# Performance work log

Hardware: AMD Instinct MI355X
Metric: run time of the kernel (lower is better)

Reference implementation:

```python
import jax, jax.numpy as jnp
import numpy as np

NUM_KEYPOINTS = 17
MAX_PEOPLE = 30
HEAT_THRESH = 0.1
KERNEL = 3  # NMS max-pool window
STRIDE_SCALE = 4  # heatmap -> image coordinate scale


def setup_inputs() -> dict:
    key = jax.random.key(0)
    # [B, C, H, W] keypoint heatmaps (values in [0,1), thresh=0.1)
    heatmaps = jax.random.uniform(key, (32, NUM_KEYPOINTS, 256, 256), dtype=jnp.float32)
    return {"heatmaps": heatmaps}


def reference(heatmaps):
    """Batched equivalent of PosePostProcessor: max-pool NMS + threshold + top-k.

    Returns fixed-shape (padded) results instead of variable-length Python lists:
      kps:    [B, C, MAX_PEOPLE, 2] int32, (x, y) * 4 image coords (sorted by score desc)
      scores: [B, C, MAX_PEOPLE] float32, 0 where invalid
      valid:  [B, C, MAX_PEOPLE] bool, True where score > heat_thresh
    """
    B, C, H, W = heatmaps.shape
    # 3x3 stride-1 SAME max pool (NMS): keep only local maxima
    hmax = jax.lax.reduce_window(
        heatmaps, -jnp.inf, jax.lax.max,
        window_dimensions=(1, 1, KERNEL, KERNEL),
        window_strides=(1, 1, 1, 1),
        padding="SAME",
    )
    nms = jnp.where(hmax == heatmaps, heatmaps, jnp.zeros((), heatmaps.dtype))
    # per (b, c) top-k over flattened spatial dims; suppress sub-threshold peaks
    flat = nms.reshape(B, C, H * W)
    masked = jnp.where(flat > HEAT_THRESH, flat, -jnp.inf)
    scores, idx = jax.lax.top_k(masked, MAX_PEOPLE)  # [B, C, K]
    x = (idx % W) * STRIDE_SCALE
    y = (idx // W) * STRIDE_SCALE
    kps = jnp.stack([x, y], axis=-1).astype(jnp.int32)  # [B, C, K, 2]
    valid = scores > HEAT_THRESH
    scores = jnp.where(valid, scores, jnp.zeros((), scores.dtype))
    return kps, scores, valid
```

## Files before the change

### kernel.cpp

```cpp
#include <hip/hip_runtime.h>
#include <cstdint>

#define HEAT_THRESH 0.1f
#define STATIC_T 0.998f
#define WW 256
#define HH 256
#define TOPK 30
#define CAPQ 128
#define NBINS 2048
#define CAP2 512
#define BASEBITS 0x3DCCCCCDu
#define BINSH 14
#define MAXBIN 1740

typedef unsigned long long u64;

__device__ __forceinline__ u64 umax64(u64 a, u64 b) { return a > b ? a : b; }

__global__ __launch_bounds__(256, 4) void nms_scan(const float* __restrict__ heat,
                                                   u64* __restrict__ cand,
                                                   int* __restrict__ cntq) {
    const int blk = blockIdx.x;
    const int slice = blk >> 2;
    const int q = blk & 3;
    const float* __restrict__ hm = heat + (size_t)slice * (HH * WW);
    const int tid = threadIdx.x;
    const int lane = tid & 63;
    const int x0 = lane * 4;
    const int y0 = q * 64 + (tid >> 6) * 16;
    const float NEG = -INFINITY;
    const float4 NEG4 = make_float4(NEG, NEG, NEG, NEG);

    __shared__ u64 cl[CAPQ];
    __shared__ int lcnt;
    if (tid == 0) lcnt = 0;
    __syncthreads();

    auto hmaxs = [&](const float4& v, float4& h) {
        float l = __shfl_up(v.w, 1u, 64);
        float r = __shfl_down(v.x, 1u, 64);
        if (lane == 0) l = NEG;
        if (lane == 63) r = NEG;
        h.x = fmaxf(fmaxf(l, v.x), v.y);
        h.y = fmaxf(fmaxf(v.x, v.y), v.z);
        h.z = fmaxf(fmaxf(v.y, v.z), v.w);
        h.w = fmaxf(fmaxf(v.z, v.w), r);
    };

    float4 r[18];
    #pragma unroll
    for (int j = 0; j < 18; ++j) {
        int y = y0 - 1 + j;
        y = (y < 0) ? 0 : ((y > HH - 1) ? HH - 1 : y);
        r[j] = *reinterpret_cast<const float4*>(hm + y * WW + x0);
    }
    __builtin_amdgcn_sched_barrier(0);
    if (y0 == 0)       r[0]  = NEG4;
    if (y0 + 16 == HH) r[17] = NEG4;

    float4 h0, h1, h2;
    hmaxs(r[0], h0);
    hmaxs(r[1], h1);
    #pragma unroll
    for (int t = 0; t < 16; ++t) {
        hmaxs(r[t + 2], h2);
        const float4 c = r[t + 1];
        const float va0 = fmaxf(fmaxf(h0.x, h1.x), h2.x);
        const float va1 = fmaxf(fmaxf(h0.y, h1.y), h2.y);
        const float va2 = fmaxf(fmaxf(h0.z, h1.z), h2.z);
        const float va3 = fmaxf(fmaxf(h0.w, h1.w), h2.w);
        const int ib = (y0 + t) * WW + x0;
        #define PUSH(cv, va, off)                                                       \
            if ((cv) == (va) && (cv) >= STATIC_T) {                                     \
                int p = atomicAdd(&lcnt, 1);                                            \
                if (p < CAPQ)                                                           \
                    cl[p] = ((u64)__float_as_uint(cv) << 32) |                          \
                            (u64)(0xFFFFu - (unsigned)(ib + (off)));                    \
            }
        PUSH(c.x, va0, 0)
        PUSH(c.y, va1, 1)
        PUSH(c.z, va2, 2)
        PUSH(c.w, va3, 3)
        #undef PUSH
        h0 = h1; h1 = h2;
    }
    __syncthreads();

    const int n = lcnt;
    if (tid == 0) cntq[blk] = n;
    const int nf = min(n, CAPQ);
    for (int i = tid; i < nf; i += 256) cand[(size_t)blk * CAPQ + i] = cl[i];
}

__global__ __launch_bounds__(64, 8) void select_topk(const float* __restrict__ heat,
                                                     const u64* __restrict__ cand,
                                                     const int* __restrict__ cntq,
                                                     float* __restrict__ out, int BC) {
    const int slice = blockIdx.x;
    const int lane = threadIdx.x;
    const float NEG = -INFINITY;
    const float4 NEG4 = make_float4(NEG, NEG, NEG, NEG);

    __shared__ unsigned hist[NBINS];
    __shared__ u64 c2[CAP2];
    __shared__ int cnt2_s;
    __shared__ unsigned tb_s;

    const int n0 = cntq[slice * 4 + 0];
    const int n1 = cntq[slice * 4 + 1];
    const int n2 = cntq[slice * 4 + 2];
    const int n3 = cntq[slice * 4 + 3];
    const bool ok = (n0 <= CAPQ) && (n1 <= CAPQ) && (n2 <= CAPQ) && (n3 <= CAPQ) &&
                    (n0 + n1 + n2 + n3 >= TOPK);

    u64 loc[8];
    #pragma unroll
    for (int j = 0; j < 8; ++j) loc[j] = 0ull;

    if (ok) {
        const int nq[4] = {n0, n1, n2, n3};
        #pragma unroll
        for (int qq = 0; qq < 4; ++qq) {
            const u64* src = cand + (size_t)(slice * 4 + qq) * CAPQ;
            if (lane < nq[qq])      loc[2 * qq]     = src[lane];
            if (lane + 64 < nq[qq]) loc[2 * qq + 1] = src[lane + 64];
        }
    } else {
        const float* __restrict__ hm = heat + (size_t)slice * (HH * WW);
        const int x0 = lane * 4;
        auto ld = [&](int y) { return *reinterpret_cast<const float4*>(hm + y * WW + x0); };
        auto hmaxs = [&](const float4& v, float4& h) {
            float l = __shfl_up(v.w, 1u, 64);
            float r = __shfl_down(v.x, 1u, 64);
            if (lane == 0) l = NEG;
            if (lane == 63) r = NEG;
            h.x = fmaxf(fmaxf(l, v.x), v.y);
            h.y = fmaxf(fmaxf(v.x, v.y), v.z);
            h.z = fmaxf(fmaxf(v.y, v.z), v.w);
            h.w = fmaxf(fmaxf(v.z, v.w), r);
        };
        for (int i = lane; i < NBINS; i += 64) hist[i] = 0u;
        if (lane == 0) cnt2_s = 0;
        __syncthreads();
        {
            float4 hmA = NEG4, hmB, cB, vN;
            cB = ld(0); hmaxs(cB, hmB);
            vN = ld(1);
            for (int y = 0; y < HH; ++y) {
                float4 hmC; hmaxs(vN, hmC);
                const float4 vNN = (y + 2 < HH) ? ld(y + 2) : NEG4;
                const float va0 = fmaxf(fmaxf(hmA.x, hmB.x), hmC.x);
                const float va1 = fmaxf(fmaxf(hmA.y, hmB.y), hmC.y);
                const float va2 = fmaxf(fmaxf(hmA.z, hmB.z), hmC.z);
                const float va3 = fmaxf(fmaxf(hmA.w, hmB.w), hmC.w);
                if (cB.x == va0 && cB.x > HEAT_THRESH) atomicAdd(&hist[(__float_as_uint(cB.x) - BASEBITS) >> BINSH], 1u);
                if (cB.y == va1 && cB.y > HEAT_THRESH) atomicAdd(&hist[(__float_as_uint(cB.y) - BASEBITS) >> BINSH], 1u);
                if (cB.z == va2 && cB.z > HEAT_THRESH) atomicAdd(&hist[(__float_as_uint(cB.z) - BASEBITS) >> BINSH], 1u);
                if (cB.w == va3 && cB.w > HEAT_THRESH) atomicAdd(&hist[(__float_as_uint(cB.w) - BASEBITS) >> BINSH], 1u);
                hmA = hmB; hmB = hmC; cB = vN; vN = vNN;
            }
        }
        __syncthreads();
        if (lane == 0) {
            unsigned cum = 0; int b;
            for (b = MAXBIN; b >= 0; --b) { cum += hist[b]; if (cum >= TOPK) break; }
            if (b < 0) b = 0;
            tb_s = BASEBITS + ((unsigned)b << BINSH);
        }
        __syncthreads();
        const unsigned tb = tb_s;
        {
            float4 hmA = NEG4, hmB, cB, vN;
            cB = ld(0); hmaxs(cB, hmB);
            vN = ld(1);
            for (int y = 0; y < HH; ++y) {
                float4 hmC; hmaxs(vN, hmC);
                const float4 vNN = (y + 2 < HH) ? ld(y + 2) : NEG4;
                const float va0 = fmaxf(fmaxf(hmA.x, hmB.x), hmC.x);
                const float va1 = fmaxf(fmaxf(hmA.y, hmB.y), hmC.y);
                const float va2 = fmaxf(fmaxf(hmA.z, hmB.z), hmC.z);
                const float va3 = fmaxf(fmaxf(hmA.w, hmB.w), hmC.w);
                const int ib = y * WW + x0;
                #define PUSHF(c, va, off)                                                   \
                    if ((c) == (va) && (c) > HEAT_THRESH && __float_as_uint(c) >= tb) {     \
                        int p = atomicAdd(&cnt2_s, 1);                                      \
                        if (p < CAP2)                                                       \
                            c2[p] = ((u64)__float_as_uint(c) << 32) |                       \
                                    (u64)(0xFFFFu - (unsigned)(ib + (off)));                \
                    }
                PUSHF(cB.x, va0, 0)
                PUSHF(cB.y, va1, 1)
                PUSHF(cB.z, va2, 2)
                PUSHF(cB.w, va3, 3)
                #undef PUSHF
                hmA = hmB; hmB = hmC; cB = vN; vN = vNN;
            }
        }
        __syncthreads();
        const int nn = min(cnt2_s, CAP2);
        #pragma unroll
        for (int j = 0; j < 8; ++j) {
            const int i = lane + 64 * j;
            if (i < nn) loc[j] = c2[i];
        }
    }

    u64 lmax = 0ull;
    #pragma unroll
    for (int j = 0; j < 8; ++j) lmax = umax64(lmax, loc[j]);

    for (int k = 0; k < TOPK; ++k) {
        u64 wm = lmax;
        #pragma unroll
        for (int s = 32; s; s >>= 1)
            wm = umax64(wm, (u64)__shfl_xor((long long)wm, s, 64));
        if (lane == 0) {
            const size_t bk = (size_t)slice * TOPK + k;
            const size_t nbk = (size_t)BC * TOPK;
            if (wm != 0ull) {
                const unsigned fb = (unsigned)(wm >> 32);
                const unsigned idx = 0xFFFFu - (unsigned)(wm & 0xFFFFFFFFull);
                out[bk * 2]       = (float)((idx & 255) * 4);
                out[bk * 2 + 1]   = (float)((idx >> 8) * 4);
                out[nbk * 2 + bk] = __uint_as_float(fb);
                out[nbk * 3 + bk] = 1.0f;
            } else {
                out[bk * 2] = 0.0f; out[bk * 2 + 1] = 0.0f;
                out[nbk * 2 + bk] = 0.0f; out[nbk * 3 + bk] = 0.0f;
            }
        }
        if (wm != 0ull && lmax == wm) {
            u64 nl = 0ull;
            #pragma unroll
            for (int j = 0; j < 8; ++j) {
                if (loc[j] == wm) loc[j] = 0ull;
                nl = umax64(nl, loc[j]);
            }
            lmax = nl;
        }
    }
}

extern "C" void kernel_launch(void* const* d_in, const int* in_sizes, int n_in,
                              void* d_out, int out_size, void* d_ws, size_t ws_size,
                              hipStream_t stream) {
    const float* heat = (const float*)d_in[0];
    float* out = (float*)d_out;
    const int BC = in_sizes[0] / (HH * WW);
    u64* cand = (u64*)d_ws;
    int* cntq = (int*)((char*)d_ws + (size_t)BC * 4 * CAPQ * sizeof(u64));
    hipLaunchKernelGGL(nms_scan, dim3(BC * 4), dim3(256), 0, stream, heat, cand, cntq);
    hipLaunchKernelGGL(select_topk, dim3(BC), dim3(64), 0, stream, heat, cand, cntq, out, BC);
}
```

Baseline: 47.73 us.

## Use per-wave stripes with ballot compaction and a persistent grid in NMS scan

Each wave now owns an independent 16-row stripe and writes its candidates straight to global memory. Positions come from ballot/popcount compaction instead of a shared-memory atomic counter and a block barrier. The grid is a fixed 1024 blocks that loop over stripes. The top-k kernel now reads 16 per-stripe counts and up to 16 candidate registers per lane. This removes LDS atomics and __syncthreads, at the cost of more register pressure in select_topk and smaller per-stripe capacity (32), which could trigger the slow fallback path more often.

New measurement: 53.49 us. 1.12x slower.

```diff
diff --git a/kernel.cpp b/kernel.cpp
--- a/kernel.cpp
+++ b/kernel.cpp
@@ -6,7 +6,7 @@
 #define WW 256
 #define HH 256
 #define TOPK 30
-#define CAPQ 128
+#define CAPB 32
 #define NBINS 2048
 #define CAP2 512
 #define BASEBITS 0x3DCCCCCDu
@@ -19,22 +19,15 @@
 
 __global__ __launch_bounds__(256, 4) void nms_scan(const float* __restrict__ heat,
                                                    u64* __restrict__ cand,
-                                                   int* __restrict__ cntq) {
-    const int blk = blockIdx.x;
-    const int slice = blk >> 2;
-    const int q = blk & 3;
-    const float* __restrict__ hm = heat + (size_t)slice * (HH * WW);
+                                                   int* __restrict__ cntb,
+                                                   int nstripes) {
     const int tid = threadIdx.x;
     const int lane = tid & 63;
+    const int nw = gridDim.x * 4;
+    const int gw = blockIdx.x * 4 + (tid >> 6);
     const int x0 = lane * 4;
-    const int y0 = q * 64 + (tid >> 6) * 16;
     const float NEG = -INFINITY;
     const float4 NEG4 = make_float4(NEG, NEG, NEG, NEG);
-
-    __shared__ u64 cl[CAPQ];
-    __shared__ int lcnt;
-    if (tid == 0) lcnt = 0;
-    __syncthreads();
 
     auto hmaxs = [&](const float4& v, float4& h) {
         float l = __shfl_up(v.w, 1u, 64);
@@ -47,54 +40,59 @@
         h.w = fmaxf(fmaxf(v.z, v.w), r);
     };
 
-    float4 r[18];
-    #pragma unroll
-    for (int j = 0; j < 18; ++j) {
-        int y = y0 - 1 + j;
-        y = (y < 0) ? 0 : ((y > HH - 1) ? HH - 1 : y);
-        r[j] = *reinterpret_cast<const float4*>(hm + y * WW + x0);
-    }
-    __builtin_amdgcn_sched_barrier(0);
-    if (y0 == 0)       r[0]  = NEG4;
-    if (y0 + 16 == HH) r[17] = NEG4;
-
-    float4 h0, h1, h2;
-    hmaxs(r[0], h0);
-    hmaxs(r[1], h1);
-    #pragma unroll
-    for (int t = 0; t < 16; ++t) {
-        hmaxs(r[t + 2], h2);
-        const float4 c = r[t + 1];
-        const float va0 = fmaxf(fmaxf(h0.x, h1.x), h2.x);
-        const float va1 = fmaxf(fmaxf(h0.y, h1.y), h2.y);
-        const float va2 = fmaxf(fmaxf(h0.z, h1.z), h2.z);
-        const float va3 = fmaxf(fmaxf(h0.w, h1.w), h2.w);
-        const int ib = (y0 + t) * WW + x0;
-        #define PUSH(cv, va, off)                                                       \
-            if ((cv) == (va) && (cv) >= STATIC_T) {                                     \
-                int p = atomicAdd(&lcnt, 1);                                            \
-                if (p < CAPQ)                                                           \
-                    cl[p] = ((u64)__float_as_uint(cv) << 32) |                          \
-                            (u64)(0xFFFFu - (unsigned)(ib + (off)));                    \
-            }
-        PUSH(c.x, va0, 0)
-        PUSH(c.y, va1, 1)
-        PUSH(c.z, va2, 2)
-        PUSH(c.w, va3, 3)
-        #undef PUSH
-        h0 = h1; h1 = h2;
-    }
-    __syncthreads();
-
-    const int n = lcnt;
-    if (tid == 0) cntq[blk] = n;
-    const int nf = min(n, CAPQ);
-    for (int i = tid; i < nf; i += 256) cand[(size_t)blk * CAPQ + i] = cl[i];
+    for (int s = gw; s < nstripes; s += nw) {
+        const int slice = s >> 4;
+        const int y0 = (s & 15) << 4;
+        const float* __restrict__ hm = heat + (size_t)slice * (HH * WW);
+
+        float4 r[18];
+        #pragma unroll
+        for (int j = 0; j < 18; ++j) {
+            int y = y0 - 1 + j;
+            y = (y < 0) ? 0 : ((y > HH - 1) ? HH - 1 : y);
+            r[j] = *reinterpret_cast<const float4*>(hm + y * WW + x0);
+        }
+        if (y0 == 0)       r[0]  = NEG4;
+        if (y0 + 16 == HH) r[17] = NEG4;
+
+        u64* __restrict__ dst = cand + (size_t)s * CAPB;
+        int wbase = 0;
+        float4 h0, h1, h2;
+        hmaxs(r[0], h0);
+        hmaxs(r[1], h1);
+        #pragma unroll
+        for (int t = 0; t < 16; ++t) {
+            hmaxs(r[t + 2], h2);
+            const float4 c = r[t + 1];
+            const int ib = (y0 + t) * WW + x0;
+            #define PUSH(cv, va, off)                                                   \
+                {                                                                       \
+                    const bool isc = ((cv) == (va)) && ((cv) >= STATIC_T);              \
+                    const u64 m = __ballot(isc);                                        \
+                    if (m) {                                                            \
+                        if (isc) {                                                      \
+                            const int pos = wbase + __popcll(m & ((1ull << lane) - 1ull)); \
+                            if (pos < CAPB)                                             \
+                                dst[pos] = ((u64)__float_as_uint(cv) << 32) |           \
+                                           (u64)(0xFFFFu - (unsigned)(ib + (off)));     \
+                        }                                                               \
+                        wbase += __popcll(m);                                           \
+                    }                                                                   \
+                }
+            PUSH(c.x, fmaxf(fmaxf(h0.x, h1.x), h2.x), 0)
+            PUSH(c.y, fmaxf(fmaxf(h0.y, h1.y), h2.y), 1)
+            PUSH(c.z, fmaxf(fmaxf(h0.z, h1.z), h2.z), 2)
+            PUSH(c.w, fmaxf(fmaxf(h0.w, h1.w), h2.w), 3)
+            #undef PUSH
+            h0 = h1; h1 = h2;
+        }
+        if (lane == 0) cntb[s] = wbase;
+    }
 }
 
 __global__ __launch_bounds__(64, 8) void select_topk(const float* __restrict__ heat,
                                                      const u64* __restrict__ cand,
-                                                     const int* __restrict__ cntq,
+                                                     const int* __restrict__ cntb,
                                                      float* __restrict__ out, int BC) {
     const int slice = blockIdx.x;
     const int lane = threadIdx.x;
@@ -106,24 +104,26 @@
     __shared__ int cnt2_s;
     __shared__ unsigned tb_s;
 
-    const int n0 = cntq[slice * 4 + 0];
-    const int n1 = cntq[slice * 4 + 1];
-    const int n2 = cntq[slice * 4 + 2];
-    const int n3 = cntq[slice * 4 + 3];
-    const bool ok = (n0 <= CAPQ) && (n1 <= CAPQ) && (n2 <= CAPQ) && (n3 <= CAPQ) &&
-                    (n0 + n1 + n2 + n3 >= TOPK);
-
-    u64 loc[8];
+    int nb[16];
+    bool ok = true;
+    int tot = 0;
     #pragma unroll
-    for (int j = 0; j < 8; ++j) loc[j] = 0ull;
+    for (int j = 0; j < 16; ++j) {
+        nb[j] = cntb[slice * 16 + j];
+        ok = ok && (nb[j] <= CAPB);
+        tot += nb[j];
+    }
+    ok = ok && (tot >= TOPK);
+
+    u64 loc[16];
+    #pragma unroll
+    for (int j = 0; j < 16; ++j) loc[j] = 0ull;
 
     if (ok) {
-        const int nq[4] = {n0, n1, n2, n3};
-        #pragma unroll
-        for (int qq = 0; qq < 4; ++qq) {
-            const u64* src = cand + (size_t)(slice * 4 + qq) * CAPQ;
-            if (lane < nq[qq])      loc[2 * qq]     = src[lane];
-            if (lane + 64 < nq[qq]) loc[2 * qq + 1] = src[lane + 64];
+        #pragma unroll
+        for (int j = 0; j < 16; ++j) {
+            if (lane < nb[j])
+                loc[j] = cand[(size_t)(slice * 16 + j) * CAPB + lane];
         }
     } else {
         const float* __restrict__ hm = heat + (size_t)slice * (HH * WW);
@@ -207,7 +207,7 @@
 
     u64 lmax = 0ull;
     #pragma unroll
-    for (int j = 0; j < 8; ++j) lmax = umax64(lmax, loc[j]);
+    for (int j = 0; j < 16; ++j) lmax = umax64(lmax, loc[j]);
 
     for (int k = 0; k < TOPK; ++k) {
         u64 wm = lmax;
@@ -232,7 +232,7 @@
         if (wm != 0ull && lmax == wm) {
             u64 nl = 0ull;
             #pragma unroll
-            for (int j = 0; j < 8; ++j) {
+            for (int j = 0; j < 16; ++j) {
                 if (loc[j] == wm) loc[j] = 0ull;
                 nl = umax64(nl, loc[j]);
             }
@@ -248,7 +248,9 @@
     float* out = (float*)d_out;
     const int BC = in_sizes[0] / (HH * WW);
     u64* cand = (u64*)d_ws;
-    int* cntq = (int*)((char*)d_ws + (size_t)BC * 4 * CAPQ * sizeof(u64));
-    hipLaunchKernelGGL(nms_scan, dim3(BC * 4), dim3(256), 0, stream, heat, cand, cntq);
-    hipLaunchKernelGGL(select_topk, dim3(BC), dim3(64), 0, stream, heat, cand, cntq, out, BC);
+    int* cntb = (int*)((char*)d_ws + (size_t)BC * 16 * CAPB * sizeof(u64));
+    hipLaunchKernelGGL(nms_scan, dim3(1024), dim3(256), 0, stream,
+                       heat, cand, cntb, BC * 16);
+    hipLaunchKernelGGL(select_topk, dim3(BC), dim3(64), 0, stream,
+                       heat, cand, cntb, out, BC);
 }
```
